# Performance work log

Hardware: AMD Instinct MI355X
Metric: run time of the kernel (lower is better)

Reference implementation:

```python
import jax, jax.numpy as jnp
import numpy as np

V, D, NH, L, T, B = 32000, 1024, 16, 6, 1024, 2
HS = D // NH
EPS = 1e-5


def setup_inputs() -> dict:
    key = jax.random.key(0)
    ks = jax.random.split(key, 20)
    s = 0.02
    inp = {
        'tokens': jax.random.randint(ks[0], (B, T), 0, V),
        'tok_emb': jax.random.normal(ks[1], (V, D), jnp.float32) * s,
        'pos_emb': jax.random.normal(ks[2], (T, D), jnp.float32) * s,
        'Wq': jax.random.normal(ks[3], (L, D, NH, HS), jnp.float32) * s,
        'Wk': jax.random.normal(ks[4], (L, D, NH, HS), jnp.float32) * s,
        'Wv': jax.random.normal(ks[5], (L, D, NH, HS), jnp.float32) * s,
        'Wo': jax.random.normal(ks[6], (L, D, D), jnp.float32) * s,
        'bo': jnp.zeros((L, D), jnp.float32),
        'ln1_s': jnp.ones((L, D), jnp.float32),
        'ln1_b': jnp.zeros((L, D), jnp.float32),
        'ln2_s': jnp.ones((L, D), jnp.float32),
        'ln2_b': jnp.zeros((L, D), jnp.float32),
        'W1': jax.random.normal(ks[7], (L, D, 4 * D), jnp.float32) * s,
        'b1': jnp.zeros((L, 4 * D), jnp.float32),
        'W2': jax.random.normal(ks[8], (L, 4 * D, D), jnp.float32) * s,
        'b2': jnp.zeros((L, D), jnp.float32),
        'lnf_s': jnp.ones((D,), jnp.float32),
        'lnf_b': jnp.zeros((D,), jnp.float32),
        'Wlm': jax.random.normal(ks[9], (D, V), jnp.float32) * s,
        'blm': jnp.zeros((V,), jnp.float32),
    }
    return inp


def _layernorm(x, scale, bias):
    m = jnp.mean(x, axis=-1, keepdims=True)
    v = jnp.mean(jnp.square(x - m), axis=-1, keepdims=True)
    return (x - m) * jax.lax.rsqrt(v + EPS) * scale + bias


def reference(tokens, tok_emb, pos_emb, Wq, Wk, Wv, Wo, bo,
              ln1_s, ln1_b, ln2_s, ln2_b, W1, b1, W2, b2,
              lnf_s, lnf_b, Wlm, blm):
    x = tok_emb[tokens] + pos_emb[None, :, :]  # [B,T,D]
    causal = jnp.tril(jnp.ones((T, T), bool))
    scale = HS ** -0.5
    for l in range(L):
        h = _layernorm(x, ln1_s[l], ln1_b[l])
        q = jnp.einsum('btd,dhe->bhte', h, Wq[l])
        k = jnp.einsum('btd,dhe->bhte', h, Wk[l])
        v = jnp.einsum('btd,dhe->bhte', h, Wv[l])
        wei = jnp.einsum('bhqe,bhke->bhqk', q, k) * scale
        wei = jnp.where(causal, wei, -jnp.inf)
        wei = jax.nn.softmax(wei, axis=-1)
        attn = jnp.einsum('bhqk,bhke->bhqe', wei, v)  # [B,NH,T,HS]
        attn = attn.transpose(0, 2, 1, 3).reshape(B, T, D)
        x = x + attn @ Wo[l] + bo[l]
        h = _layernorm(x, ln2_s[l], ln2_b[l])
        x = x + jax.nn.relu(h @ W1[l] + b1[l]) @ W2[l] + b2[l]
    x = _layernorm(x, lnf_s, lnf_b)
    logits = x @ Wlm + blm  # [B,T,V]
    return logits
```

## Files before the change

kernel.cpp:

```cpp
#include <hip/hip_runtime.h>
#include <hip/hip_bf16.h>
#include <stdint.h>

#define L_LAYERS 6
#define D_MODEL  1024
#define N_HEAD   16
#define H_SZ     64
#define T_SEQ    1024
#define B_BATCH  2
#define M_ROWS   2048
#define V_VOCAB  32000

typedef __attribute__((ext_vector_type(8))) short bf16x8;
typedef __attribute__((ext_vector_type(4))) short bf16x4;
typedef __attribute__((ext_vector_type(4))) float floatx4;

static __device__ __forceinline__ short f2bf(float f) {
  __hip_bfloat16 h = __float2bfloat16(f);
  return *reinterpret_cast<short*>(&h);
}

static __device__ __forceinline__ void lds_cp16(const void* g, void* l) {
  __builtin_amdgcn_global_load_lds(
      (const __attribute__((address_space(1))) uint32_t*)g,
      (__attribute__((address_space(3))) uint32_t*)l, 16, 0, 0);
}

#define WVM(n) asm volatile("s_waitcnt vmcnt(" #n ")" ::: "memory")
#define BARR __builtin_amdgcn_s_barrier()

__global__ __launch_bounds__(256) void transpose_cvt(const float* __restrict__ in,
                                                     short* __restrict__ out,
                                                     int R, int C,
                                                     long in_stride, long out_stride) {
  in  += (size_t)blockIdx.z * in_stride;
  out += (size_t)blockIdx.z * out_stride;
  __shared__ float tile[64][65];
  int rt = blockIdx.x, ct = blockIdx.y;
  int tid = threadIdx.x;
  int r0 = tid >> 4;
  int c0 = (tid & 15) << 2;
  const float* ip = in + (size_t)(rt * 64) * C + ct * 64;
#pragma unroll
  for (int p = 0; p < 4; ++p) {
    int r = r0 + (p << 4);
    float4 v = *(const float4*)(ip + (size_t)r * C + c0);
    tile[r][c0] = v.x; tile[r][c0 + 1] = v.y; tile[r][c0 + 2] = v.z; tile[r][c0 + 3] = v.w;
  }
  __syncthreads();
  short* op = out + (size_t)(ct * 64) * R + rt * 64;
#pragma unroll
  for (int p = 0; p < 4; ++p) {
    int c = r0 + (p << 4);
    bf16x4 s;
    s.x = f2bf(tile[c0 + 0][c]);
    s.y = f2bf(tile[c0 + 1][c]);
    s.z = f2bf(tile[c0 + 2][c]);
    s.w = f2bf(tile[c0 + 3][c]);
    *(bf16x4*)(op + (size_t)c * R + c0) = s;
  }
}

__global__ __launch_bounds__(256) void embed_kernel(const int* __restrict__ tokens,
                                                    const float* __restrict__ tok_emb,
                                                    const float* __restrict__ pos_emb,
                                                    float* __restrict__ x) {
  int row = blockIdx.x;
  int t = row & 1023;
  int tok = tokens[row];
  int c = threadIdx.x << 2;
  float4 e = *(const float4*)(tok_emb + (size_t)tok * 1024 + c);
  float4 p = *(const float4*)(pos_emb + (size_t)t * 1024 + c);
  float4 rr; rr.x = e.x + p.x; rr.y = e.y + p.y; rr.z = e.z + p.z; rr.w = e.w + p.w;
  *(float4*)(x + (size_t)row * 1024 + c) = rr;
}

__global__ __launch_bounds__(256) void ln_kernel(const float* __restrict__ xin,
                                                 const float* __restrict__ sc,
                                                 const float* __restrict__ bi,
                                                 short* __restrict__ out) {
  int row = blockIdx.x, tid = threadIdx.x;
  int c = tid << 2;
  float4 v = *(const float4*)(xin + (size_t)row * 1024 + c);
  float s = v.x + v.y + v.z + v.w;
  float q = v.x * v.x + v.y * v.y + v.z * v.z + v.w * v.w;
#pragma unroll
  for (int off = 32; off > 0; off >>= 1) {
    s += __shfl_xor(s, off);
    q += __shfl_xor(q, off);
  }
  __shared__ float rs[4], rq[4];
  if ((tid & 63) == 0) { rs[tid >> 6] = s; rq[tid >> 6] = q; }
  __syncthreads();
  s = rs[0] + rs[1] + rs[2] + rs[3];
  q = rq[0] + rq[1] + rq[2] + rq[3];
  float mean = s * (1.f / 1024.f);
  float var = q * (1.f / 1024.f) - mean * mean;
  float rstd = rsqrtf(var + 1e-5f);
  float4 g = *(const float4*)(sc + c);
  float4 bb = *(const float4*)(bi + c);
  bf16x4 o4;
  o4.x = f2bf((v.x - mean) * rstd * g.x + bb.x);
  o4.y = f2bf((v.y - mean) * rstd * g.y + bb.y);
  o4.z = f2bf((v.z - mean) * rstd * g.z + bb.z);
  o4.w = f2bf((v.w - mean) * rstd * g.w + bb.w);
  *(bf16x4*)(out + (size_t)row * 1024 + c) = o4;
}

template <bool BIAS, bool RELU, bool RESID, bool OUTBF16>
__global__ __launch_bounds__(256) void gemm3_kernel(const short* __restrict__ A,
                                                    const short* __restrict__ Bt,
                                                    const float* __restrict__ bias,
                                                    const float* __restrict__ resid,
                                                    void* __restrict__ Cout,
                                                    int K, int N) {
  constexpr int ABY = 64 * 128;
  constexpr int BBY = 128 * 128;
  extern __shared__ char smem[];
  char* Asm = smem;
  char* Bsm = smem + 3 * ABY;
  const int NB = N >> 7;
  int nwg = 32 * NB;
  int bid = blockIdx.x;
  int wgid = (bid & 7) * (nwg >> 3) + (bid >> 3);
  int bn = wgid >> 5, bm = wgid & 31;
  int tid = threadIdx.x;
  int lane = tid & 63, w = tid >> 6;
  int lr = lane & 15, lg = lane >> 4;
  int wn = w & 1, wm = w >> 1;

  const floatx4 FZ = {0.f, 0.f, 0.f, 0.f};
  floatx4 acc[2][4];
#pragma unroll
  for (int m = 0; m < 2; ++m)
#pragma unroll
    for (int n = 0; n < 4; ++n) acc[m][n] = FZ;

  size_t aoff[2], boff[4];
  {
    int rr = tid >> 3;
    int g = (tid & 7) ^ (rr & 7);
#pragma unroll
    for (int i = 0; i < 2; ++i)
      aoff[i] = (size_t)(bm * 64 + i * 32 + rr) * K + g * 8;
#pragma unroll
    for (int i = 0; i < 4; ++i)
      boff[i] = (size_t)(bn * 128 + i * 32 + rr) * K + g * 8;
  }

#define STA3(b, k0)                                                        \
  _Pragma("unroll") for (int i = 0; i < 2; ++i)                            \
    lds_cp16(A + aoff[i] + (k0), Asm + (b) * ABY + i * 4096 + tid * 16);
#define STB3(b, k0)                                                        \
  _Pragma("unroll") for (int i = 0; i < 4; ++i)                            \
    lds_cp16(Bt + boff[i] + (k0), Bsm + (b) * BBY + i * 4096 + tid * 16);
#define LDA3(b, kh)                                                        \
  _Pragma("unroll") for (int f = 0; f < 2; ++f) {                          \
    int lrow = wm * 32 + f * 16 + lr;                                      \
    af[f] = *(const bf16x8*)(Asm + (b) * ABY + lrow * 128 +                \
                             (((((kh) << 2) + lg) ^ (lrow & 7)) << 4));    \
  }
#define LDB3(b, kh)                                                        \
  _Pragma("unroll") for (int n = 0; n < 4; ++n) {                          \
    int lcol = wn * 64 + n * 16 + lr;                                      \
    bfr[n] = *(const bf16x8*)(Bsm + (b) * BBY + lcol * 128 +               \
                              (((((kh) << 2) + lg) ^ (lcol & 7)) << 4));   \
  }
#define MFMA3                                                              \
  __builtin_amdgcn_s_setprio(1);                                           \
  _Pragma("unroll") for (int f = 0; f < 2; ++f)                            \
  _Pragma("unroll") for (int n = 0; n < 4; ++n)                            \
    acc[f][n] = __builtin_amdgcn_mfma_f32_16x16x32_bf16(af[f], bfr[n],     \
                                                        acc[f][n], 0, 0, 0);\
  __builtin_amdgcn_s_setprio(0);

  const int nt = K >> 6;
  STA3(0, 0); STB3(0, 0);
  STA3(1, 64); STB3(1, 64);
  WVM(6);
  BARR;

  int cbuf = 0, sbuf = 2;
  for (int t = 0; t < nt; ++t) {
    bf16x8 af[2], bfr[4];
    bool pre = (t + 2 < nt);
    int k2 = (t + 2) << 6;
    if (pre) { STA3(sbuf, k2); }
    LDA3(cbuf, 0); LDB3(cbuf, 0);
    MFMA3;
    if (pre) { STB3(sbuf, k2); }
    LDA3(cbuf, 1); LDB3(cbuf, 1);
    MFMA3;
    if (pre) { WVM(6); } else { WVM(0); }
    BARR;
    cbuf = (cbuf == 2) ? 0 : cbuf + 1;
    sbuf = (sbuf == 2) ? 0 : sbuf + 1;
  }

#pragma unroll
  for (int n = 0; n < 4; ++n) {
    int col = (bn << 7) + wn * 64 + (n << 4) + lr;
    float bv = 0.f;
    if (BIAS) bv = bias[col];
#pragma unroll
    for (int m = 0; m < 2; ++m) {
      int row0 = bm * 64 + wm * 32 + (m << 4) + (lg << 2);
#pragma unroll
      for (int r = 0; r < 4; ++r) {
        size_t idx = (size_t)(row0 + r) * N + col;
        float val = acc[m][n][r] + bv;
        if (RESID) val += resid[idx];
        if (RELU) val = fmaxf(val, 0.f);
        if (OUTBF16) ((short*)Cout)[idx] = f2bf(val);
        else ((float*)Cout)[idx] = val;
      }
    }
  }
#undef STA3
#undef STB3
#undef LDA3
#undef LDB3
#undef MFMA3
}

template <bool BIAS, bool OUTBF16>
__global__ __launch_bounds__(512) void gemm8_kernel(const short* __restrict__ A,
                                                    const short* __restrict__ Bt,
                                                    const float* __restrict__ bias,
                                                    void* __restrict__ Cout,
                                                    int K, int N) {
  extern __shared__ char smem[];
  char* Asm = smem;
  char* Bsm = smem + 65536;
  const int NB = N >> 8;
  int nwg = 8 * NB;
  int bid = blockIdx.x;
  int wgid = (bid & 7) * (nwg >> 3) + (bid >> 3);
  int bm = wgid & 7, bn = wgid >> 3;
  int tid = threadIdx.x;
  int lane = tid & 63, w = tid >> 6;
  int lr = lane & 15, lg = lane >> 4;
  int wm = w >> 2, wn = w & 3;

  const floatx4 FZ = {0.f, 0.f, 0.f, 0.f};
  floatx4 acc[8][4];
#pragma unroll
  for (int m = 0; m < 8; ++m)
#pragma unroll
    for (int n = 0; n < 4; ++n) acc[m][n] = FZ;

  size_t aoff[2][2], boff[4];
  {
    int rr = tid >> 3;
    int g = (tid & 7) ^ (rr & 7);
#pragma unroll
    for (int c = 0; c < 2; ++c)
#pragma unroll
      for (int i = 0; i < 2; ++i) {
        int lrow = i * 64 + rr;
        int grow = (lrow & 63) + ((lrow >> 6) << 7) + (c << 6);
        aoff[c][i] = (size_t)(bm * 256 + grow) * K + g * 8;
      }
#pragma unroll
    for (int i = 0; i < 4; ++i)
      boff[i] = (size_t)(bn * 256 + i * 64 + rr) * K + g * 8;
  }

  bf16x8 areg[4], breg[2][4];

#define LDA8(chunk, kh)                                                          \
  _Pragma("unroll") for (int f = 0; f < 4; ++f) {                                \
    int lrow = wm * 64 + f * 16 + lr;                                            \
    areg[f] = *(const bf16x8*)(Asm + buf * 32768 + (chunk) * 16384 + lrow * 128  \
                               + (((((kh) << 2) + lg) ^ (lrow & 7)) << 4));      \
  }
#define LDB8(kh)                                                                 \
  _Pragma("unroll") for (int n = 0; n < 4; ++n) {                                \
    int lcol = wn * 64 + n * 16 + lr;                                            \
    breg[kh][n] = *(const bf16x8*)(Bsm + buf * 32768 + lcol * 128                \
                                   + (((((kh) << 2) + lg) ^ (lcol & 7)) << 4));  \
  }
#define MFMA16(mh, kh)                                                           \
  __builtin_amdgcn_s_setprio(1);                                                 \
  _Pragma("unroll") for (int f = 0; f < 4; ++f)                                  \
  _Pragma("unroll") for (int n = 0; n < 4; ++n)                                  \
    acc[(mh) * 4 + f][n] = __builtin_amdgcn_mfma_f32_16x16x32_bf16(              \
        areg[f], breg[kh][n], acc[(mh) * 4 + f][n], 0, 0, 0);                    \
  __builtin_amdgcn_s_setprio(0);
#define STA8(chunk, dstbuf, k0)                                                  \
  _Pragma("unroll") for (int i = 0; i < 2; ++i)                                  \
    lds_cp16(A + aoff[chunk][i] + (k0),                                          \
             Asm + (dstbuf) * 32768 + (chunk) * 16384 + i * 8192 + tid * 16);
#define STB8(dstbuf, k0)                                                         \
  _Pragma("unroll") for (int i = 0; i < 4; ++i)                                  \
    lds_cp16(Bt + boff[i] + (k0),                                                \
             Bsm + (dstbuf) * 32768 + i * 8192 + tid * 16);

  const int nt = K >> 6;
  STA8(0, 0, 0); STB8(0, 0); STA8(1, 0, 0);
  WVM(2);
  BARR;

  int buf = 0;
  for (int t = 0; t < nt - 1; ++t) {
    int k1 = (t + 1) << 6;
    int ob = buf ^ 1;
    LDA8(0, 0); LDB8(0);
    STA8(0, ob, k1);
    BARR;
    MFMA16(0, 0);
    BARR;
    LDA8(0, 1); LDB8(1);
    STB8(ob, k1);
    WVM(6);
    BARR;
    MFMA16(0, 1);
    BARR;
    LDA8(1, 0);
    STA8(1, ob, k1);
    BARR;
    MFMA16(1, 0);
    BARR;
    LDA8(1, 1);
    WVM(2);
    BARR;
    MFMA16(1, 1);
    BARR;
    buf ^= 1;
  }
  LDA8(0, 0); LDB8(0);
  MFMA16(0, 0);
  LDA8(0, 1); LDB8(1);
  MFMA16(0, 1);
  WVM(0);
  BARR;
  LDA8(1, 0);
  MFMA16(1, 0);
  LDA8(1, 1);
  MFMA16(1, 1);

#pragma unroll
  for (int n = 0; n < 4; ++n) {
    int col = (bn << 8) + (wn << 6) + (n << 4) + lr;
    float bv = 0.f;
    if (BIAS) bv = bias[col];
#pragma unroll
    for (int m = 0; m < 8; ++m) {
      int row0 = (bm << 8) + (wm << 7) + (m << 4) + (lg << 2);
#pragma unroll
      for (int r = 0; r < 4; ++r) {
        size_t idx = (size_t)(row0 + r) * N + col;
        float val = acc[m][n][r] + bv;
        if (OUTBF16) ((short*)Cout)[idx] = f2bf(val);
        else ((float*)Cout)[idx] = val;
      }
    }
  }
#undef LDA8
#undef LDB8
#undef MFMA16
#undef STA8
#undef STB8
}

__global__ __launch_bounds__(256) void vt_kernel(const short* __restrict__ qkv,
                                                 short* __restrict__ vt) {
  int bh = blockIdx.x, tt = blockIdx.y;
  int b = bh >> 4, hh = bh & 15;
  __shared__ short tile[64][68];
  int tid = threadIdx.x;
  int r0 = tid >> 4;
  int c4 = (tid & 15) << 2;
  const short* ip = qkv + (size_t)((b << 10) + (tt << 6)) * 3072 + 2048 + (hh << 6);
#pragma unroll
  for (int p = 0; p < 4; ++p) {
    int t = r0 + (p << 4);
    bf16x4 v = *(const bf16x4*)(ip + (size_t)t * 3072 + c4);
    tile[t][c4] = v.x; tile[t][c4 + 1] = v.y; tile[t][c4 + 2] = v.z; tile[t][c4 + 3] = v.w;
  }
  __syncthreads();
  short* op = vt + (size_t)(bh << 6) * 1024 + (tt << 6);
#pragma unroll
  for (int p = 0; p < 4; ++p) {
    int e = r0 + (p << 4);
    bf16x4 sv;
    sv.x = tile[c4 + 0][e];
    sv.y = tile[c4 + 1][e];
    sv.z = tile[c4 + 2][e];
    sv.w = tile[c4 + 3][e];
    *(bf16x4*)(op + (size_t)e * 1024 + c4) = sv;
  }
}

__global__ __launch_bounds__(256) void attn_kernel(const short* __restrict__ qkv,
                                                   const short* __restrict__ vt,
                                                   short* __restrict__ out) {
  int bh = blockIdx.x;
  int qt = blockIdx.y;
  int b = bh >> 4, hh = bh & 15;
  int tid = threadIdx.x;
  int lane = tid & 63, w = tid >> 6;
  int lr = lane & 15, lg = lane >> 4;

  __shared__ short Ks[64 * 64];
  __shared__ short Vs[64 * 64];
  __shared__ short Ps[4][16 * 68];

  const floatx4 FZ = {0.f, 0.f, 0.f, 0.f};
  const short* qb = qkv + (size_t)((b << 10) + (qt << 6) + (w << 4) + lr) * 3072 + (hh << 6);
  bf16x8 qf0 = *(const bf16x8*)(qb + (lg << 3));
  bf16x8 qf1 = *(const bf16x8*)(qb + 32 + (lg << 3));

  floatx4 o[4];
  float mrun[4], lrun[4];
#pragma unroll
  for (int r = 0; r < 4; ++r) { o[r] = FZ; mrun[r] = -3e38f; lrun[r] = 0.f; }

  int sr = lane >> 3;
  int cb = (lane & 7) << 4;
  int csw = cb ^ (sr << 4);
  const short* kB = qkv + (size_t)(b << 10) * 3072 + 1024 + (hh << 6);
  const short* vB = vt + (size_t)(bh << 6) * 1024;

  for (int jt = 0; jt <= qt; ++jt) {
    __syncthreads();
#pragma unroll
    for (int j = 0; j < 2; ++j) {
      int ch = w * 2 + j;
      int row = (ch << 3) + sr;
      lds_cp16(kB + (size_t)((jt << 6) + row) * 3072 + (csw >> 1), (short*)Ks + (ch << 9));
      lds_cp16(vB + (size_t)row * 1024 + (jt << 6) + (csw >> 1), (short*)Vs + (ch << 9));
    }
    __syncthreads();

    const char* KsB = (const char*)Ks;
    const char* VsB = (const char*)Vs;
    floatx4 s[4];
#pragma unroll
    for (int f = 0; f < 4; ++f) {
      int rk = (f << 4) + lr;
      int sw = (rk & 7) << 4;
      bf16x8 kf0 = *(const bf16x8*)(KsB + rk * 128 + ((lg << 4) ^ sw));
      bf16x8 kf1 = *(const bf16x8*)(KsB + rk * 128 + ((64 + (lg << 4)) ^ sw));
      floatx4 t = __builtin_amdgcn_mfma_f32_16x16x32_bf16(qf0, kf0, FZ, 0, 0, 0);
      s[f] = __builtin_amdgcn_mfma_f32_16x16x32_bf16(qf1, kf1, t, 0, 0, 0);
    }

    float p[4][4], mt[4];
    bool diag = (jt == qt);
    int rowloc = (w << 4) + (lg << 2);
#pragma unroll
    for (int r = 0; r < 4; ++r) {
      float m = -3e38f;
#pragma unroll
      for (int f = 0; f < 4; ++f) {
        float sv = s[f][r] * 0.125f;
        if (diag && ((f << 4) + lr > rowloc + r)) sv = -3e38f;
        p[f][r] = sv;
        m = fmaxf(m, sv);
      }
      mt[r] = m;
    }
#pragma unroll
    for (int off = 1; off < 16; off <<= 1) {
#pragma unroll
      for (int r = 0; r < 4; ++r) mt[r] = fmaxf(mt[r], __shfl_xor(mt[r], off));
    }
    float corr[4], psum[4];
#pragma unroll
    for (int r = 0; r < 4; ++r) {
      float mnew = fmaxf(mrun[r], mt[r]);
      corr[r] = __expf(mrun[r] - mnew);
      mrun[r] = mnew;
      float ps = 0.f;
#pragma unroll
      for (int f = 0; f < 4; ++f) {
        float e = __expf(p[f][r] - mnew);
        p[f][r] = e;
        ps += e;
      }
      psum[r] = ps;
    }
#pragma unroll
    for (int off = 1; off < 16; off <<= 1) {
#pragma unroll
      for (int r = 0; r < 4; ++r) psum[r] += __shfl_xor(psum[r], off);
    }
    floatx4 cv;
#pragma unroll
    for (int r = 0; r < 4; ++r) { lrun[r] = lrun[r] * corr[r] + psum[r]; cv[r] = corr[r]; }
#pragma unroll
    for (int f = 0; f < 4; ++f) o[f] *= cv;

    char* PsB = (char*)&Ps[w][0];
#pragma unroll
    for (int f = 0; f < 4; ++f)
#pragma unroll
      for (int r = 0; r < 4; ++r)
        *(short*)(PsB + ((lg << 2) + r) * 136 + (((f << 4) + lr) << 1)) = f2bf(p[f][r]);

#pragma unroll
    for (int kk = 0; kk < 2; ++kk) {
      const char* pb = PsB + lr * 136 + (kk << 6) + (lg << 4);
      union { struct { bf16x4 lo, hi; } h2; bf16x8 v; } pu;
      pu.h2.lo = *(const bf16x4*)pb;
      pu.h2.hi = *(const bf16x4*)(pb + 8);
      bf16x8 pa = pu.v;
#pragma unroll
      for (int f = 0; f < 4; ++f) {
        int rv = (f << 4) + lr;
        int sw = (rv & 7) << 4;
        bf16x8 vf = *(const bf16x8*)(VsB + rv * 128 + ((((kk << 6)) + (lg << 4)) ^ sw));
        o[f] = __builtin_amdgcn_mfma_f32_16x16x32_bf16(pa, vf, o[f], 0, 0, 0);
      }
    }
  }

#pragma unroll
  for (int f = 0; f < 4; ++f) {
#pragma unroll
    for (int r = 0; r < 4; ++r) {
      int row = (qt << 6) + (w << 4) + (lg << 2) + r;
      int col = (hh << 6) + (f << 4) + lr;
      out[(size_t)((b << 10) + row) * 1024 + col] = f2bf(o[f][r] / lrun[r]);
    }
  }
}

extern "C" void kernel_launch(void* const* d_in, const int* in_sizes, int n_in,
                              void* d_out, int out_size, void* d_ws, size_t ws_size,
                              hipStream_t stream) {
  const int*   tokens  = (const int*)d_in[0];
  const float* tok_emb = (const float*)d_in[1];
  const float* pos_emb = (const float*)d_in[2];
  const float* Wq  = (const float*)d_in[3];
  const float* Wk  = (const float*)d_in[4];
  const float* Wv  = (const float*)d_in[5];
  const float* Wo  = (const float*)d_in[6];
  const float* bo  = (const float*)d_in[7];
  const float* ln1s = (const float*)d_in[8];
  const float* ln1b = (const float*)d_in[9];
  const float* ln2s = (const float*)d_in[10];
  const float* ln2b = (const float*)d_in[11];
  const float* W1  = (const float*)d_in[12];
  const float* b1  = (const float*)d_in[13];
  const float* W2  = (const float*)d_in[14];
  const float* b2  = (const float*)d_in[15];
  const float* lnfs = (const float*)d_in[16];
  const float* lnfb = (const float*)d_in[17];
  const float* Wlm = (const float*)d_in[18];
  const float* blm = (const float*)d_in[19];

  short* wqkvT = (short*)d_ws;
  short* woT   = wqkvT + (size_t)L_LAYERS * 3072 * 1024;
  short* w1T   = woT   + (size_t)L_LAYERS * 1024 * 1024;
  short* w2T   = w1T   + (size_t)L_LAYERS * 4096 * 1024;
  short* wlmT  = w2T   + (size_t)L_LAYERS * 1024 * 4096;
  float* x     = (float*)(wlmT + (size_t)V_VOCAB * 1024);
  short* h     = (short*)(x + (size_t)M_ROWS * 1024);
  short* qkv   = h + (size_t)M_ROWS * 1024;
  short* vtb   = qkv + (size_t)M_ROWS * 3072;
  short* attnb = vtb + (size_t)B_BATCH * N_HEAD * H_SZ * T_SEQ;
  short* mid   = attnb + (size_t)M_ROWS * 1024;

  dim3 blk(256, 1, 1);

  (void)hipFuncSetAttribute(reinterpret_cast<const void*>(&gemm8_kernel<true, false>),
                            hipFuncAttributeMaxDynamicSharedMemorySize, 131072);
  (void)hipFuncSetAttribute(reinterpret_cast<const void*>(&gemm3_kernel<false, false, false, true>),
                            hipFuncAttributeMaxDynamicSharedMemorySize, 73728);
  (void)hipFuncSetAttribute(reinterpret_cast<const void*>(&gemm3_kernel<true, false, true, false>),
                            hipFuncAttributeMaxDynamicSharedMemorySize, 73728);
  (void)hipFuncSetAttribute(reinterpret_cast<const void*>(&gemm3_kernel<true, true, false, true>),
                            hipFuncAttributeMaxDynamicSharedMemorySize, 73728);

  transpose_cvt<<<dim3(16, 16, 6), blk, 0, stream>>>(Wq, wqkvT,             1024, 1024, 1048576, 3072 * 1024);
  transpose_cvt<<<dim3(16, 16, 6), blk, 0, stream>>>(Wk, wqkvT + 1048576,   1024, 1024, 1048576, 3072 * 1024);
  transpose_cvt<<<dim3(16, 16, 6), blk, 0, stream>>>(Wv, wqkvT + 2097152,   1024, 1024, 1048576, 3072 * 1024);
  transpose_cvt<<<dim3(16, 16, 6), blk, 0, stream>>>(Wo, woT,               1024, 1024, 1048576, 1048576);
  transpose_cvt<<<dim3(16, 64, 6), blk, 0, stream>>>(W1, w1T,               1024, 4096, 4194304, 4194304);
  transpose_cvt<<<dim3(64, 16, 6), blk, 0, stream>>>(W2, w2T,               4096, 1024, 4194304, 4194304);
  transpose_cvt<<<dim3(16, 500, 1), blk, 0, stream>>>(Wlm, wlmT,            1024, V_VOCAB, 0, 0);

  embed_kernel<<<M_ROWS, blk, 0, stream>>>(tokens, tok_emb, pos_emb, x);

  for (int l = 0; l < L_LAYERS; ++l) {
    ln_kernel<<<M_ROWS, blk, 0, stream>>>(x, ln1s + l * 1024, ln1b + l * 1024, h);
    gemm3_kernel<false, false, false, true><<<32 * 24, blk, 73728, stream>>>(
        h, wqkvT + (size_t)l * 3072 * 1024, nullptr, nullptr, qkv, 1024, 3072);
    vt_kernel<<<dim3(32, 16), blk, 0, stream>>>(qkv, vtb);
    attn_kernel<<<dim3(32, 16), blk, 0, stream>>>(qkv, vtb, attnb);
    gemm3_kernel<true, false, true, false><<<32 * 8, blk, 73728, stream>>>(
        attnb, woT + (size_t)l * 1048576, bo + l * 1024, x, x, 1024, 1024);
    ln_kernel<<<M_ROWS, blk, 0, stream>>>(x, ln2s + l * 1024, ln2b + l * 1024, h);
    gemm3_kernel<true, true, false, true><<<32 * 32, blk, 73728, stream>>>(
        h, w1T + (size_t)l * 4194304, b1 + l * 4096, nullptr, mid, 1024, 4096);
    gemm3_kernel<true, false, true, false><<<32 * 8, blk, 73728, stream>>>(
        mid, w2T + (size_t)l * 4194304, b2 + l * 1024, x, x, 4096, 1024);
  }

  ln_kernel<<<M_ROWS, blk, 0, stream>>>(x, lnfs, lnfb, h);
  gemm8_kernel<true, false><<<dim3(8 * 125), dim3(512, 1, 1), 131072, stream>>>(
      h, wlmT, blm, (float*)d_out, 1024, V_VOCAB);
}
```

Measured before the change: 1.210 ms.

## Split-K the N=1024 GEMMs, fuse residual reduction into layernorm, widen FFN1 tiles

The Wo and W2 projections (N=1024) now use a split-K=2 kernel that writes two fp32 partial sums. This doubles the workgroup count from 256 to 512 so more CUs are busy. A new lnred kernel adds both partials, the bias and the residual into x, then applies layernorm in the same pass, replacing the separate residual epilogue. FFN1 moves to a 128x256 tile kernel with 512 threads and 144KB of LDS. The cost is extra fp32 partial traffic and lower occupancy per CU for FFN1.

```diff
diff --git a/kernel.cpp b/kernel.cpp
--- a/kernel.cpp
+++ b/kernel.cpp
@@ -82,6 +82,50 @@
   int row = blockIdx.x, tid = threadIdx.x;
   int c = tid << 2;
   float4 v = *(const float4*)(xin + (size_t)row * 1024 + c);
+  float s = v.x + v.y + v.z + v.w;
+  float q = v.x * v.x + v.y * v.y + v.z * v.z + v.w * v.w;
+#pragma unroll
+  for (int off = 32; off > 0; off >>= 1) {
+    s += __shfl_xor(s, off);
+    q += __shfl_xor(q, off);
+  }
+  __shared__ float rs[4], rq[4];
+  if ((tid & 63) == 0) { rs[tid >> 6] = s; rq[tid >> 6] = q; }
+  __syncthreads();
+  s = rs[0] + rs[1] + rs[2] + rs[3];
+  q = rq[0] + rq[1] + rq[2] + rq[3];
+  float mean = s * (1.f / 1024.f);
+  float var = q * (1.f / 1024.f) - mean * mean;
+  float rstd = rsqrtf(var + 1e-5f);
+  float4 g = *(const float4*)(sc + c);
+  float4 bb = *(const float4*)(bi + c);
+  bf16x4 o4;
+  o4.x = f2bf((v.x - mean) * rstd * g.x + bb.x);
+  o4.y = f2bf((v.y - mean) * rstd * g.y + bb.y);
+  o4.z = f2bf((v.z - mean) * rstd * g.z + bb.z);
+  o4.w = f2bf((v.w - mean) * rstd * g.w + bb.w);
+  *(bf16x4*)(out + (size_t)row * 1024 + c) = o4;
+}
+
+__global__ __launch_bounds__(256) void lnred_kernel(float* __restrict__ xio,
+                                                    const float* __restrict__ P0,
+                                                    const float* __restrict__ P1,
+                                                    const float* __restrict__ gb,
+                                                    const float* __restrict__ sc,
+                                                    const float* __restrict__ bi,
+                                                    short* __restrict__ out) {
+  int row = blockIdx.x, tid = threadIdx.x;
+  int c = tid << 2;
+  size_t base = (size_t)row * 1024 + c;
+  float4 v = *(const float4*)(xio + base);
+  float4 p0 = *(const float4*)(P0 + base);
+  float4 p1 = *(const float4*)(P1 + base);
+  float4 gv = *(const float4*)(gb + c);
+  v.x += p0.x + p1.x + gv.x;
+  v.y += p0.y + p1.y + gv.y;
+  v.z += p0.z + p1.z + gv.z;
+  v.w += p0.w + p1.w + gv.w;
+  *(float4*)(xio + base) = v;
   float s = v.x + v.y + v.z + v.w;
   float q = v.x * v.x + v.y * v.y + v.z * v.z + v.w * v.w;
 #pragma unroll
@@ -221,6 +265,229 @@
 #undef LDA3
 #undef LDB3
 #undef MFMA3
+}
+
+__global__ __launch_bounds__(256) void gemm3sk_kernel(const short* __restrict__ A,
+                                                      const short* __restrict__ Bt,
+                                                      float* __restrict__ Pout,
+                                                      int K, int N) {
+  constexpr int ABY = 64 * 128;
+  constexpr int BBY = 128 * 128;
+  extern __shared__ char smem[];
+  char* Asm = smem;
+  char* Bsm = smem + 3 * ABY;
+  const int NB = N >> 7;
+  int nwg = 64 * NB;
+  int bid = blockIdx.x;
+  int wgid = (bid & 7) * (nwg >> 3) + (bid >> 3);
+  int half = wgid >= (nwg >> 1);
+  int w2 = wgid - half * (nwg >> 1);
+  int bn = w2 >> 5, bm = w2 & 31;
+  int kbase = half * (K >> 1);
+  Pout += (size_t)half * M_ROWS * N;
+  int tid = threadIdx.x;
+  int lane = tid & 63, w = tid >> 6;
+  int lr = lane & 15, lg = lane >> 4;
+  int wn = w & 1, wm = w >> 1;
+
+  const floatx4 FZ = {0.f, 0.f, 0.f, 0.f};
+  floatx4 acc[2][4];
+#pragma unroll
+  for (int m = 0; m < 2; ++m)
+#pragma unroll
+    for (int n = 0; n < 4; ++n) acc[m][n] = FZ;
+
+  size_t aoff[2], boff[4];
+  {
+    int rr = tid >> 3;
+    int g = (tid & 7) ^ (rr & 7);
+#pragma unroll
+    for (int i = 0; i < 2; ++i)
+      aoff[i] = (size_t)(bm * 64 + i * 32 + rr) * K + kbase + g * 8;
+#pragma unroll
+    for (int i = 0; i < 4; ++i)
+      boff[i] = (size_t)(bn * 128 + i * 32 + rr) * K + kbase + g * 8;
+  }
+
+#define STA3(b, k0)                                                        \
+  _Pragma("unroll") for (int i = 0; i < 2; ++i)                            \
+    lds_cp16(A + aoff[i] + (k0), Asm + (b) * ABY + i * 4096 + tid * 16);
+#define STB3(b, k0)                                                        \
+  _Pragma("unroll") for (int i = 0; i < 4; ++i)                            \
+    lds_cp16(Bt + boff[i] + (k0), Bsm + (b) * BBY + i * 4096 + tid * 16);
+#define LDA3(b, kh)                                                        \
+  _Pragma("unroll") for (int f = 0; f < 2; ++f) {                          \
+    int lrow = wm * 32 + f * 16 + lr;                                      \
+    af[f] = *(const bf16x8*)(Asm + (b) * ABY + lrow * 128 +                \
+                             (((((kh) << 2) + lg) ^ (lrow & 7)) << 4));    \
+  }
+#define LDB3(b, kh)                                                        \
+  _Pragma("unroll") for (int n = 0; n < 4; ++n) {                          \
+    int lcol = wn * 64 + n * 16 + lr;                                      \
+    bfr[n] = *(const bf16x8*)(Bsm + (b) * BBY + lcol * 128 +               \
+                              (((((kh) << 2) + lg) ^ (lcol & 7)) << 4));   \
+  }
+#define MFMA3                                                              \
+  __builtin_amdgcn_s_setprio(1);                                           \
+  _Pragma("unroll") for (int f = 0; f < 2; ++f)                            \
+  _Pragma("unroll") for (int n = 0; n < 4; ++n)                            \
+    acc[f][n] = __builtin_amdgcn_mfma_f32_16x16x32_bf16(af[f], bfr[n],     \
+                                                        acc[f][n], 0, 0, 0);\
+  __builtin_amdgcn_s_setprio(0);
+
+  const int nt = (K >> 1) >> 6;
+  STA3(0, 0); STB3(0, 0);
+  STA3(1, 64); STB3(1, 64);
+  WVM(6);
+  BARR;
+
+  int cbuf = 0, sbuf = 2;
+  for (int t = 0; t < nt; ++t) {
+    bf16x8 af[2], bfr[4];
+    bool pre = (t + 2 < nt);
+    int k2 = (t + 2) << 6;
+    if (pre) { STA3(sbuf, k2); }
+    LDA3(cbuf, 0); LDB3(cbuf, 0);
+    MFMA3;
+    if (pre) { STB3(sbuf, k2); }
+    LDA3(cbuf, 1); LDB3(cbuf, 1);
+    MFMA3;
+    if (pre) { WVM(6); } else { WVM(0); }
+    BARR;
+    cbuf = (cbuf == 2) ? 0 : cbuf + 1;
+    sbuf = (sbuf == 2) ? 0 : sbuf + 1;
+  }
+
+#pragma unroll
+  for (int n = 0; n < 4; ++n) {
+    int col = (bn << 7) + wn * 64 + (n << 4) + lr;
+#pragma unroll
+    for (int m = 0; m < 2; ++m) {
+      int row0 = bm * 64 + wm * 32 + (m << 4) + (lg << 2);
+#pragma unroll
+      for (int r = 0; r < 4; ++r)
+        Pout[(size_t)(row0 + r) * N + col] = acc[m][n][r];
+    }
+  }
+#undef STA3
+#undef STB3
+#undef LDA3
+#undef LDB3
+#undef MFMA3
+}
+
+template <bool BIAS, bool RELU, bool OUTBF16>
+__global__ __launch_bounds__(512) void gemmw_kernel(const short* __restrict__ A,
+                                                    const short* __restrict__ Bt,
+                                                    const float* __restrict__ bias,
+                                                    void* __restrict__ Cout,
+                                                    int K, int N) {
+  constexpr int ABY = 128 * 128;
+  constexpr int BBY = 256 * 128;
+  extern __shared__ char smem[];
+  char* Asm = smem;
+  char* Bsm = smem + 3 * ABY;
+  const int NB = N >> 8;
+  int nwg = 16 * NB;
+  int bid = blockIdx.x;
+  int wgid = (bid & 7) * (nwg >> 3) + (bid >> 3);
+  int bn = wgid >> 4, bm = wgid & 15;
+  int tid = threadIdx.x;
+  int lane = tid & 63, w = tid >> 6;
+  int lr = lane & 15, lg = lane >> 4;
+  int wm = w >> 2, wn = w & 3;
+
+  const floatx4 FZ = {0.f, 0.f, 0.f, 0.f};
+  floatx4 acc[4][4];
+#pragma unroll
+  for (int m = 0; m < 4; ++m)
+#pragma unroll
+    for (int n = 0; n < 4; ++n) acc[m][n] = FZ;
+
+  size_t aoff[2], boff[4];
+  {
+    int rr = tid >> 3;
+    int g = (tid & 7) ^ (rr & 7);
+#pragma unroll
+    for (int i = 0; i < 2; ++i)
+      aoff[i] = (size_t)(bm * 128 + i * 64 + rr) * K + g * 8;
+#pragma unroll
+    for (int i = 0; i < 4; ++i)
+      boff[i] = (size_t)(bn * 256 + i * 64 + rr) * K + g * 8;
+  }
+
+#define STAW(b, k0)                                                        \
+  _Pragma("unroll") for (int i = 0; i < 2; ++i)                            \
+    lds_cp16(A + aoff[i] + (k0), Asm + (b) * ABY + i * 8192 + tid * 16);
+#define STBW(b, k0)                                                        \
+  _Pragma("unroll") for (int i = 0; i < 4; ++i)                            \
+    lds_cp16(Bt + boff[i] + (k0), Bsm + (b) * BBY + i * 8192 + tid * 16);
+#define LDAW(b, kh)                                                        \
+  _Pragma("unroll") for (int f = 0; f < 4; ++f) {                          \
+    int lrow = wm * 64 + f * 16 + lr;                                      \
+    af[f] = *(const bf16x8*)(Asm + (b) * ABY + lrow * 128 +                \
+                             (((((kh) << 2) + lg) ^ (lrow & 7)) << 4));    \
+  }
+#define LDBW(b, kh)                                                        \
+  _Pragma("unroll") for (int n = 0; n < 4; ++n) {                          \
+    int lcol = wn * 64 + n * 16 + lr;                                      \
+    bfr[n] = *(const bf16x8*)(Bsm + (b) * BBY + lcol * 128 +               \
+                              (((((kh) << 2) + lg) ^ (lcol & 7)) << 4));   \
+  }
+#define MFMAW                                                              \
+  __builtin_amdgcn_s_setprio(1);                                           \
+  _Pragma("unroll") for (int f = 0; f < 4; ++f)                            \
+  _Pragma("unroll") for (int n = 0; n < 4; ++n)                            \
+    acc[f][n] = __builtin_amdgcn_mfma_f32_16x16x32_bf16(af[f], bfr[n],     \
+                                                        acc[f][n], 0, 0, 0);\
+  __builtin_amdgcn_s_setprio(0);
+
+  const int nt = K >> 6;
+  STAW(0, 0); STBW(0, 0);
+  STAW(1, 64); STBW(1, 64);
+  WVM(6);
+  BARR;
+
+  int cbuf = 0, sbuf = 2;
+  for (int t = 0; t < nt; ++t) {
+    bf16x8 af[4], bfr[4];
+    bool pre = (t + 2 < nt);
+    int k2 = (t + 2) << 6;
+    if (pre) { STAW(sbuf, k2); }
+    LDAW(cbuf, 0); LDBW(cbuf, 0);
+    MFMAW;
+    if (pre) { STBW(sbuf, k2); }
+    LDAW(cbuf, 1); LDBW(cbuf, 1);
+    MFMAW;
+    if (pre) { WVM(6); } else { WVM(0); }
+    BARR;
+    cbuf = (cbuf == 2) ? 0 : cbuf + 1;
+    sbuf = (sbuf == 2) ? 0 : sbuf + 1;
+  }
+
+#pragma unroll
+  for (int n = 0; n < 4; ++n) {
+    int col = (bn << 8) + wn * 64 + (n << 4) + lr;
+    float bv = 0.f;
+    if (BIAS) bv = bias[col];
+#pragma unroll
+    for (int m = 0; m < 4; ++m) {
+      int row0 = bm * 128 + wm * 64 + (m << 4) + (lg << 2);
+#pragma unroll
+      for (int r = 0; r < 4; ++r) {
+        size_t idx = (size_t)(row0 + r) * N + col;
+        float val = acc[m][n][r] + bv;
+        if (RELU) val = fmaxf(val, 0.f);
+        if (OUTBF16) ((short*)Cout)[idx] = f2bf(val);
+        else ((float*)Cout)[idx] = val;
+      }
+    }
+  }
+#undef STAW
+#undef STBW
+#undef LDAW
+#undef LDBW
+#undef MFMAW
 }
 
 template <bool BIAS, bool OUTBF16>
@@ -562,6 +829,8 @@
   short* vtb   = qkv + (size_t)M_ROWS * 3072;
   short* attnb = vtb + (size_t)B_BATCH * N_HEAD * H_SZ * T_SEQ;
   short* mid   = attnb + (size_t)M_ROWS * 1024;
+  float* psum  = (float*)(mid + (size_t)M_ROWS * 4096);
+  float* psum1 = psum + (size_t)M_ROWS * 1024;
 
   dim3 blk(256, 1, 1);
 
@@ -569,10 +838,10 @@
                             hipFuncAttributeMaxDynamicSharedMemorySize, 131072);
   (void)hipFuncSetAttribute(reinterpret_cast<const void*>(&gemm3_kernel<false, false, false, true>),
                             hipFuncAttributeMaxDynamicSharedMemorySize, 73728);
-  (void)hipFuncSetAttribute(reinterpret_cast<const void*>(&gemm3_kernel<true, false, true, false>),
+  (void)hipFuncSetAttribute(reinterpret_cast<const void*>(&gemm3sk_kernel),
                             hipFuncAttributeMaxDynamicSharedMemorySize, 73728);
-  (void)hipFuncSetAttribute(reinterpret_cast<const void*>(&gemm3_kernel<true, true, false, true>),
-                            hipFuncAttributeMaxDynamicSharedMemorySize, 73728);
+  (void)hipFuncSetAttribute(reinterpret_cast<const void*>(&gemmw_kernel<true, true, true>),
+                            hipFuncAttributeMaxDynamicSharedMemorySize, 147456);
 
   transpose_cvt<<<dim3(16, 16, 6), blk, 0, stream>>>(Wq, wqkvT,             1024, 1024, 1048576, 3072 * 1024);
   transpose_cvt<<<dim3(16, 16, 6), blk, 0, stream>>>(Wk, wqkvT + 1048576,   1024, 1024, 1048576, 3072 * 1024);
@@ -585,21 +854,28 @@
   embed_kernel<<<M_ROWS, blk, 0, stream>>>(tokens, tok_emb, pos_emb, x);
 
   for (int l = 0; l < L_LAYERS; ++l) {
-    ln_kernel<<<M_ROWS, blk, 0, stream>>>(x, ln1s + l * 1024, ln1b + l * 1024, h);
+    if (l == 0) {
+      ln_kernel<<<M_ROWS, blk, 0, stream>>>(x, ln1s, ln1b, h);
+    } else {
+      lnred_kernel<<<M_ROWS, blk, 0, stream>>>(x, psum, psum1, b2 + (l - 1) * 1024,
+                                               ln1s + l * 1024, ln1b + l * 1024, h);
+    }
     gemm3_kernel<false, false, false, true><<<32 * 24, blk, 73728, stream>>>(
         h, wqkvT + (size_t)l * 3072 * 1024, nullptr, nullptr, qkv, 1024, 3072);
     vt_kernel<<<dim3(32, 16), blk, 0, stream>>>(qkv, vtb);
     attn_kernel<<<dim3(32, 16), blk, 0, stream>>>(qkv, vtb, attnb);
-    gemm3_kernel<true, false, true, false><<<32 * 8, blk, 73728, stream>>>(
-        attnb, woT + (size_t)l * 1048576, bo + l * 1024, x, x, 1024, 1024);
-    ln_kernel<<<M_ROWS, blk, 0, stream>>>(x, ln2s + l * 1024, ln2b + l * 1024, h);
-    gemm3_kernel<true, true, false, true><<<32 * 32, blk, 73728, stream>>>(
-        h, w1T + (size_t)l * 4194304, b1 + l * 4096, nullptr, mid, 1024, 4096);
-    gemm3_kernel<true, false, true, false><<<32 * 8, blk, 73728, stream>>>(
-        mid, w2T + (size_t)l * 4194304, b2 + l * 1024, x, x, 4096, 1024);
-  }
-
-  ln_kernel<<<M_ROWS, blk, 0, stream>>>(x, lnfs, lnfb, h);
+    gemm3sk_kernel<<<64 * 8, blk, 73728, stream>>>(
+        attnb, woT + (size_t)l * 1048576, psum, 1024, 1024);
+    lnred_kernel<<<M_ROWS, blk, 0, stream>>>(x, psum, psum1, bo + l * 1024,
+                                             ln2s + l * 1024, ln2b + l * 1024, h);
+    gemmw_kernel<true, true, true><<<16 * 16, dim3(512, 1, 1), 147456, stream>>>(
+        h, w1T + (size_t)l * 4194304, b1 + l * 4096, mid, 1024, 4096);
+    gemm3sk_kernel<<<64 * 8, blk, 73728, stream>>>(
+        mid, w2T + (size_t)l * 4194304, psum, 4096, 1024);
+  }
+
+  lnred_kernel<<<M_ROWS, blk, 0, stream>>>(x, psum, psum1, b2 + 5 * 1024,
+                                           lnfs, lnfb, h);
   gemm8_kernel<true, false><<<dim3(8 * 125), dim3(512, 1, 1), 131072, stream>>>(
       h, wlmT, blm, (float*)d_out, 1024, V_VOCAB);
 }
```

Measured after the change: 1.141 ms. -5.7%, faster.
